# Kernel tuning notes

Measured on AMD Instinct MI355X. Metric: run time of the kernel, lower is better.

The kernel has to match this reference:

```python
import jax, jax.numpy as jnp
import numpy as np

N = 100_000      # nodes
F_IN = 256       # input features
HID = 256        # hidden dim
C = 40           # classes
E = 1_600_000    # edges
BN_EPS = 1e-5


def setup_inputs() -> dict:
    key = jax.random.key(0)
    ks = jax.random.split(key, 8)
    x = jax.random.normal(ks[0], (N, F_IN), dtype=jnp.float32)
    edge_index = jax.random.randint(ks[1], (2, E), 0, N)
    W1 = jax.random.normal(ks[2], (F_IN, HID), dtype=jnp.float32) / np.sqrt(F_IN)
    b1 = jnp.zeros((HID,), jnp.float32)
    gamma = jnp.ones((HID,), jnp.float32)
    beta = jnp.zeros((HID,), jnp.float32)
    W2 = jax.random.normal(ks[3], (HID, C), dtype=jnp.float32) / np.sqrt(HID)
    b2 = jnp.zeros((C,), jnp.float32)
    return {"x": x, "edge_index": edge_index, "W1": W1, "b1": b1,
            "gamma": gamma, "beta": beta, "W2": W2, "b2": b2}


def _gcn_propagate(h, src, dst, norm):
    # out[dst] += norm * h[src]   (symmetric-normalized aggregation, self-loops included)
    msg = norm[:, None] * h[src]                       # [E+N, D]
    return jax.ops.segment_sum(msg, dst, num_segments=N)


def reference(x, edge_index, W1, b1, gamma, beta, W2, b2):
    loops = jnp.arange(N, dtype=edge_index.dtype)
    src = jnp.concatenate([edge_index[0], loops])      # add self-loops (PyG GCNConv)
    dst = jnp.concatenate([edge_index[1], loops])
    deg = jax.ops.segment_sum(jnp.ones_like(dst, jnp.float32), dst, num_segments=N)
    dinv = jnp.where(deg > 0, jax.lax.rsqrt(deg), 0.0)
    norm = dinv[src] * dinv[dst]

    # Layer 1: GCNConv (linear without bias -> propagate -> + bias)
    h = _gcn_propagate(x @ W1, src, dst, norm) + b1    # [N, HID]
    # BatchNorm1d over nodes (training-style batch statistics, biased variance)
    mu = h.mean(axis=0)
    var = h.var(axis=0)
    h = (h - mu) * jax.lax.rsqrt(var + BN_EPS) * gamma + beta
    h = jax.nn.relu(h)                                 # dropout is identity in eval

    # Layer 2: GCNConv -> log_softmax
    out = _gcn_propagate(h @ W2, src, dst, norm) + b2  # [N, C]
    return jax.nn.log_softmax(out, axis=1)
```

## Files before the change

### kernel.cpp

```cpp
#include <hip/hip_runtime.h>
#include <math.h>

#define N_NODES 100000
#define F_IN    256
#define HID     256
#define C_OUT   40
#define N_EDGES 1600000
#define BN_EPS  1e-5f

#define SCAN_CHUNK  1024
#define SCAN_BLOCKS ((N_NODES + SCAN_CHUNK - 1) / SCAN_CHUNK)
#define CNT_BLOCKS  ((N_EDGES + 255) / 256)
#define NPASS 8
#define DRANGE (N_NODES / NPASS)

typedef __attribute__((ext_vector_type(8))) short short8;
typedef __attribute__((ext_vector_type(8))) unsigned short ushort8v;
typedef __attribute__((ext_vector_type(4))) float f32x4;

static __device__ __forceinline__ unsigned short f2bf(float f) {
    unsigned int u = __float_as_uint(f);
    unsigned int r = u + 0x7FFFu + ((u >> 16) & 1u);
    return (unsigned short)(r >> 16);
}
static __device__ __forceinline__ float bf2f(unsigned short b) {
    return __uint_as_float(((unsigned int)b) << 16);
}

__global__ void count_dst_castw(const int* __restrict__ dst, int* cnt,
                                const float* __restrict__ W1, const float* __restrict__ W2,
                                unsigned short* __restrict__ w1t, unsigned short* __restrict__ w2t) {
    int b = blockIdx.x, t = threadIdx.x;
    if (b < CNT_BLOCKS) {
        int i = b * 256 + t;
        if (i < N_EDGES) atomicAdd(&cnt[dst[i]], 1);
    } else if (b < CNT_BLOCKS + 256) {
        int n = b - CNT_BLOCKS;
        w1t[(size_t)n * 256 + t] = f2bf(W1[(size_t)t * 256 + n]);
    } else {
        int n = b - CNT_BLOCKS - 256;
        w2t[(size_t)n * 256 + t] = (n < C_OUT) ? f2bf(W2[(size_t)t * C_OUT + n]) : (unsigned short)0;
    }
}

__global__ __launch_bounds__(256) void scan_partial(const int* __restrict__ cnt,
                                                    int* blocksum) {
    __shared__ int red[256];
    int t = threadIdx.x;
    int base = blockIdx.x * SCAN_CHUNK + t * 4;
    int s = 0;
    if (base + 3 < N_NODES) {
        int4 c = *(const int4*)(cnt + base);
        s = c.x + c.y + c.z + c.w + 4;
    } else {
        for (int q = 0; q < 4; q++) if (base + q < N_NODES) s += cnt[base + q] + 1;
    }
    red[t] = s;
    __syncthreads();
    for (int off = 128; off > 0; off >>= 1) {
        if (t < off) red[t] += red[t + off];
        __syncthreads();
    }
    if (t == 0) blocksum[blockIdx.x] = red[0];
}

__global__ __launch_bounds__(128) void scan_blocksums(const int* __restrict__ blocksum,
                                                      int* blockoff, int* rowoff) {
    __shared__ int sm[128];
    int t = threadIdx.x;
    int v = (t < SCAN_BLOCKS) ? blocksum[t] : 0;
    sm[t] = v;
    __syncthreads();
    for (int off = 1; off < 128; off <<= 1) {
        int u = (t >= off) ? sm[t - off] : 0;
        __syncthreads();
        sm[t] += u;
        __syncthreads();
    }
    if (t < SCAN_BLOCKS) blockoff[t] = sm[t] - v;
    if (t == 0) rowoff[N_NODES] = N_EDGES + N_NODES;
}

__global__ __launch_bounds__(256) void scan_write_init(const int* __restrict__ cnt,
                                                       const int* __restrict__ blockoff,
                                                       int* rowoff, float* dinv,
                                                       int* cursor, int* csr) {
    __shared__ int red[256];
    int t = threadIdx.x;
    int base = blockIdx.x * SCAN_CHUNK + t * 4;
    int c[4] = {0, 0, 0, 0};
    if (base + 3 < N_NODES) {
        int4 cc = *(const int4*)(cnt + base);
        c[0] = cc.x + 1; c[1] = cc.y + 1; c[2] = cc.z + 1; c[3] = cc.w + 1;
    } else {
        for (int q = 0; q < 4; q++) c[q] = (base + q < N_NODES) ? cnt[base + q] + 1 : 0;
    }
    int s = c[0] + c[1] + c[2] + c[3];
    red[t] = s;
    __syncthreads();
    for (int off = 1; off < 256; off <<= 1) {
        int u = (t >= off) ? red[t - off] : 0;
        __syncthreads();
        red[t] += u;
        __syncthreads();
    }
    int run = blockoff[blockIdx.x] + red[t] - s;
    for (int q = 0; q < 4; q++) {
        int idx = base + q;
        if (idx < N_NODES) {
            rowoff[idx] = run;
            dinv[idx] = rsqrtf((float)c[q]);
            csr[run] = idx;
            cursor[idx] = 1;
            run += c[q];
        }
    }
}

__global__ void scatter_mp(const int* __restrict__ src,
                           const int* __restrict__ dst,
                           const int* __restrict__ rowoff,
                           int* cursor, int* csr) {
    int p = blockIdx.x / CNT_BLOCKS;
    int e = (blockIdx.x - p * CNT_BLOCKS) * 256 + threadIdx.x;
    if (e < N_EDGES) {
        int d = dst[e];
        if (d / DRANGE == p) {
            int pos = rowoff[d] + atomicAdd(&cursor[d], 1);
            csr[pos] = src[e];
        }
    }
}

#define LDK 56
__global__ __launch_bounds__(256) void gemm1_mfma(const float* __restrict__ x,
                                                  const unsigned short* __restrict__ w1t,
                                                  const float* __restrict__ dinv,
                                                  unsigned short* __restrict__ hs, int M) {
    __shared__ unsigned short As[64][LDK];
    __shared__ unsigned short Bs[256][LDK];
    int tid = threadIdx.x;
    int wave = tid >> 6, lane = tid & 63;
    int m0 = blockIdx.x * 64;
    f32x4 acc[4][4] = {};

    int ar = tid >> 2, ac = (tid & 3) * 8;
    int brow = tid;
    int gr = m0 + ar;
    bool rowok = gr < M;
    const float* xrow = x + (size_t)gr * 256 + ac;
    const unsigned short* wrow = w1t + (size_t)brow * 256;

    float4 pa = make_float4(0.f,0.f,0.f,0.f), pb = pa;
    if (rowok) { pa = *(const float4*)(xrow); pb = *(const float4*)(xrow + 4); }
    ushort8v rb0 = *(const ushort8v*)(wrow);
    ushort8v rb1 = *(const ushort8v*)(wrow + 8);
    ushort8v rb2 = *(const ushort8v*)(wrow + 16);
    ushort8v rb3 = *(const ushort8v*)(wrow + 24);

    for (int k0 = 0; k0 < 256; k0 += 32) {
        {
            ushort8v u;
            u[0] = f2bf(pa.x); u[1] = f2bf(pa.y); u[2] = f2bf(pa.z); u[3] = f2bf(pa.w);
            u[4] = f2bf(pb.x); u[5] = f2bf(pb.y); u[6] = f2bf(pb.z); u[7] = f2bf(pb.w);
            if (!rowok) {
#pragma unroll
                for (int q = 0; q < 8; q++) u[q] = 0;
            }
            *(ushort8v*)&As[ar][ac] = u;
        }
        *(ushort8v*)&Bs[brow][0]  = rb0;
        *(ushort8v*)&Bs[brow][8]  = rb1;
        *(ushort8v*)&Bs[brow][16] = rb2;
        *(ushort8v*)&Bs[brow][24] = rb3;
        __syncthreads();
        if (k0 + 32 < 256) {
            if (rowok) {
                pa = *(const float4*)(xrow + k0 + 32);
                pb = *(const float4*)(xrow + k0 + 36);
            }
            const unsigned short* p = wrow + k0 + 32;
            rb0 = *(const ushort8v*)(p);
            rb1 = *(const ushort8v*)(p + 8);
            rb2 = *(const ushort8v*)(p + 16);
            rb3 = *(const ushort8v*)(p + 24);
        }
        int fr = lane & 15, fk = (lane >> 4) * 8;
        short8 a[4], b[4];
#pragma unroll
        for (int mt = 0; mt < 4; mt++) a[mt] = *(short8*)&As[mt * 16 + fr][fk];
#pragma unroll
        for (int nt = 0; nt < 4; nt++) b[nt] = *(short8*)&Bs[wave * 64 + nt * 16 + fr][fk];
#pragma unroll
        for (int mt = 0; mt < 4; mt++)
#pragma unroll
            for (int nt = 0; nt < 4; nt++)
                acc[mt][nt] = __builtin_amdgcn_mfma_f32_16x16x32_bf16(a[mt], b[nt], acc[mt][nt], 0, 0, 0);
        __syncthreads();
    }
    int fr = lane & 15, fg = lane >> 4;
#pragma unroll
    for (int mt = 0; mt < 4; mt++) {
#pragma unroll
        for (int r = 0; r < 4; r++) {
            int row = m0 + mt * 16 + fg * 4 + r;
            if (row < M) {
                float dv = dinv[row];
#pragma unroll
                for (int nt = 0; nt < 4; nt++) {
                    int col = wave * 64 + nt * 16 + fr;
                    hs[(size_t)row * 256 + col] = f2bf(acc[mt][nt][r] * dv);
                }
            }
        }
    }
}

__global__ __launch_bounds__(256) void agg256(const int* __restrict__ rowoff,
                                              const int* __restrict__ csr,
                                              const unsigned short* __restrict__ hs,
                                              const float* __restrict__ dinv,
                                              unsigned short* __restrict__ hagg) {
    int g = blockIdx.x * blockDim.x + threadIdx.x;
    int wid = g >> 6, lane = g & 63;
    if (wid >= N_NODES) return;
    int half = lane >> 5;
    int c8 = (lane & 31) * 8;
    int beg = rowoff[wid], end = rowoff[wid + 1];
    float acc[8] = {0.f, 0.f, 0.f, 0.f, 0.f, 0.f, 0.f, 0.f};
    int j = beg;
    for (; j + 7 < end; j += 8) {
        int sx[4];
#pragma unroll
        for (int q = 0; q < 4; q++) sx[q] = csr[j + 2 * q + half];
        ushort8v u[4];
#pragma unroll
        for (int q = 0; q < 4; q++) u[q] = *(const ushort8v*)(hs + (size_t)sx[q] * 256 + c8);
#pragma unroll
        for (int q = 0; q < 4; q++)
#pragma unroll
            for (int e = 0; e < 8; e++) acc[e] += bf2f(u[q][e]);
    }
    for (; j + 1 < end; j += 2) {
        int s = csr[j + half];
        ushort8v u = *(const ushort8v*)(hs + (size_t)s * 256 + c8);
#pragma unroll
        for (int e = 0; e < 8; e++) acc[e] += bf2f(u[e]);
    }
    if (j < end && half == 0) {
        int s = csr[j];
        ushort8v u = *(const ushort8v*)(hs + (size_t)s * 256 + c8);
#pragma unroll
        for (int e = 0; e < 8; e++) acc[e] += bf2f(u[e]);
    }
#pragma unroll
    for (int e = 0; e < 8; e++) acc[e] += __shfl_xor(acc[e], 32);
    float dv = dinv[wid];
    if (half == 0) {
        ushort8v o;
#pragma unroll
        for (int e = 0; e < 8; e++) o[e] = f2bf(acc[e] * dv);
        *(ushort8v*)(hagg + (size_t)wid * 256 + c8) = o;
    }
}

#define BNS_BLOCKS 1024
__global__ __launch_bounds__(256) void bn_stats_v(const unsigned short* __restrict__ h,
                                                  float* musum, float* sqsum) {
    int tid = threadIdx.x;
    int wave = tid >> 6, lane = tid & 63;
    int half = lane >> 5;
    int c8 = (lane & 31) * 8;
    int gw = blockIdx.x * 4 + wave;
    float s[8] = {0.f,0.f,0.f,0.f,0.f,0.f,0.f,0.f};
    float q2[8] = {0.f,0.f,0.f,0.f,0.f,0.f,0.f,0.f};
    for (int r = gw * 2 + half; r < N_NODES; r += BNS_BLOCKS * 4 * 2) {
        ushort8v u = *(const ushort8v*)(h + (size_t)r * 256 + c8);
#pragma unroll
        for (int e = 0; e < 8; e++) {
            float v = bf2f(u[e]);
            s[e] += v; q2[e] += v * v;
        }
    }
#pragma unroll
    for (int e = 0; e < 8; e++) {
        s[e]  += __shfl_xor(s[e], 32);
        q2[e] += __shfl_xor(q2[e], 32);
    }
    __shared__ float sS[4][256];
    __shared__ float sQ[4][256];
    if (half == 0) {
#pragma unroll
        for (int e = 0; e < 8; e++) { sS[wave][c8 + e] = s[e]; sQ[wave][c8 + e] = q2[e]; }
    }
    __syncthreads();
    float a = sS[0][tid] + sS[1][tid] + sS[2][tid] + sS[3][tid];
    float b = sQ[0][tid] + sQ[1][tid] + sQ[2][tid] + sQ[3][tid];
    atomicAdd(&musum[tid], a);
    atomicAdd(&sqsum[tid], b);
}

#define LDB2 264
__global__ __launch_bounds__(256) void gemm2_mfma(const unsigned short* __restrict__ hagg,
                                                  const unsigned short* __restrict__ w2t,
                                                  const float* __restrict__ musum,
                                                  const float* __restrict__ sqsum,
                                                  const float* __restrict__ gamma,
                                                  const float* __restrict__ beta,
                                                  const float* __restrict__ dinv,
                                                  unsigned short* __restrict__ g2b, int M) {
    __shared__ unsigned short w2s[48][LDB2];
    __shared__ unsigned short As[64][40];
    __shared__ float ss[256], sh[256];
    int tid = threadIdx.x;
    int wave = tid >> 6, lane = tid & 63;
    int m0 = blockIdx.x * 64;

    for (int i = tid; i < 48 * 32; i += 256) {
        int rrow = i >> 5, c8 = (i & 31) * 8;
        *(ushort8v*)&w2s[rrow][c8] = *(const ushort8v*)(w2t + (size_t)rrow * 256 + c8);
    }
    {
        const float invN = 1.0f / N_NODES;
        float m = musum[tid] * invN;
        float var = sqsum[tid] * invN - m * m;
        float s = gamma[tid] * rsqrtf(var + BN_EPS);
        ss[tid] = s;
        sh[tid] = beta[tid] - m * s;
    }

    f32x4 acc[3] = {};
    int arow = tid >> 2, ac0 = (tid & 3) * 8;
    int fr = lane & 15, fk = (lane >> 4) * 8;

    for (int k0 = 0; k0 < 256; k0 += 32) {
        __syncthreads();
        {
            int gr = m0 + arow;
            ushort8v u;
            if (gr < M) {
                u = *(const ushort8v*)(hagg + (size_t)gr * 256 + k0 + ac0);
#pragma unroll
                for (int q = 0; q < 8; q++) {
                    int col = k0 + ac0 + q;
                    float v = bf2f(u[q]);
                    v = fmaxf(v * ss[col] + sh[col], 0.0f);
                    u[q] = f2bf(v);
                }
            } else {
#pragma unroll
                for (int q = 0; q < 8; q++) u[q] = 0;
            }
            *(ushort8v*)&As[arow][ac0] = u;
        }
        __syncthreads();
        short8 a = *(short8*)&As[wave * 16 + fr][fk];
#pragma unroll
        for (int nt = 0; nt < 3; nt++) {
            short8 b = *(short8*)&w2s[nt * 16 + fr][k0 + fk];
            acc[nt] = __builtin_amdgcn_mfma_f32_16x16x32_bf16(a, b, acc[nt], 0, 0, 0);
        }
    }
    int fg = lane >> 4;
#pragma unroll
    for (int nt = 0; nt < 3; nt++) {
        int col = nt * 16 + fr;
        if (col < C_OUT) {
#pragma unroll
            for (int r = 0; r < 4; r++) {
                int row = m0 + wave * 16 + fg * 4 + r;
                if (row < M) g2b[(size_t)row * C_OUT + col] = f2bf(acc[nt][r] * dinv[row]);
            }
        }
    }
}

__global__ __launch_bounds__(256) void agg40_logsm(const int* __restrict__ rowoff,
                                                   const int* __restrict__ csr,
                                                   const unsigned short* __restrict__ g2b,
                                                   const float* __restrict__ dinv,
                                                   const float* __restrict__ b2,
                                                   float* __restrict__ out) {
    int gi = blockIdx.x * blockDim.x + threadIdx.x;
    int wid = gi >> 6, lane = gi & 63;
    if (wid >= N_NODES) return;
    int g = lane / 10;
    int k4 = lane - g * 10;
    bool gact = lane < 60;
    int beg = rowoff[wid], end = rowoff[wid + 1];
    float a4[4] = {0.f, 0.f, 0.f, 0.f};
    for (int j = beg; j < end; j += 6) {
        int jj = j + g;
        if (gact && jj < end) {
            int s = csr[jj];
            ushort4 u = *(const ushort4*)(g2b + (size_t)s * C_OUT + k4 * 4);
            a4[0] += bf2f(u.x); a4[1] += bf2f(u.y);
            a4[2] += bf2f(u.z); a4[3] += bf2f(u.w);
        }
    }
#pragma unroll
    for (int e = 0; e < 4; e++) {
        float t0 = __shfl(a4[e], lane + 30);
        a4[e] += t0;
    }
#pragma unroll
    for (int e = 0; e < 4; e++) {
        float t1 = __shfl(a4[e], lane + 10);
        float t2 = __shfl(a4[e], lane + 20);
        a4[e] += t1 + t2;
    }
    bool act = lane < 10;
    float dvd = dinv[wid];
    float v[4];
    float mloc = -INFINITY;
#pragma unroll
    for (int e = 0; e < 4; e++) {
        v[e] = act ? a4[e] * dvd + b2[k4 * 4 + e] : -INFINITY;
        mloc = fmaxf(mloc, v[e]);
    }
#pragma unroll
    for (int o = 32; o > 0; o >>= 1) mloc = fmaxf(mloc, __shfl_xor(mloc, o));
    float sloc = 0.f;
    if (act) {
#pragma unroll
        for (int e = 0; e < 4; e++) sloc += __expf(v[e] - mloc);
    }
#pragma unroll
    for (int o = 32; o > 0; o >>= 1) sloc += __shfl_xor(sloc, o);
    float ls = __logf(sloc);
    if (act) {
        float4 o4 = make_float4(v[0] - mloc - ls, v[1] - mloc - ls,
                                v[2] - mloc - ls, v[3] - mloc - ls);
        *(float4*)(out + (size_t)wid * C_OUT + k4 * 4) = o4;
    }
}

extern "C" void kernel_launch(void* const* d_in, const int* in_sizes, int n_in,
                              void* d_out, int out_size, void* d_ws, size_t ws_size,
                              hipStream_t stream) {
    const float* x     = (const float*)d_in[0];
    const int*   ei    = (const int*)  d_in[1];
    const float* W1    = (const float*)d_in[2];
    const float* gamma = (const float*)d_in[4];
    const float* beta  = (const float*)d_in[5];
    const float* W2    = (const float*)d_in[6];
    const float* b2    = (const float*)d_in[7];
    float* out = (float*)d_out;

    const int* src = ei;
    const int* dst = ei + N_EDGES;

    unsigned short* hs    = (unsigned short*)d_ws;
    unsigned short* hagg  = hs + (size_t)N_NODES * 256;
    unsigned short* g2b   = hagg + (size_t)N_NODES * 256;
    float*          dinv  = (float*)(g2b + (size_t)N_NODES * C_OUT);
    int*            cnt   = (int*)(dinv + N_NODES);
    int*            rowoff= cnt + N_NODES;
    int*            cursor= rowoff + N_NODES + 1;
    int*            csr   = cursor + N_NODES;
    unsigned short* w1t   = (unsigned short*)(csr + N_EDGES + N_NODES);
    unsigned short* w2t   = w1t + 65536;
    float*          musum = (float*)(w2t + 48 * 256);
    float*          sqsum = musum + 256;
    int*            blocksum = (int*)(sqsum + 256);
    int*            blockoff = blocksum + 128;

    hipMemsetAsync(cnt, 0, N_NODES * sizeof(int), stream);
    hipMemsetAsync(musum, 0, 512 * sizeof(float), stream);

    count_dst_castw<<<CNT_BLOCKS + 256 + 48, 256, 0, stream>>>(dst, cnt, W1, W2, w1t, w2t);
    scan_partial<<<SCAN_BLOCKS, 256, 0, stream>>>(cnt, blocksum);
    scan_blocksums<<<1, 128, 0, stream>>>(blocksum, blockoff, rowoff);
    scan_write_init<<<SCAN_BLOCKS, 256, 0, stream>>>(cnt, blockoff, rowoff, dinv, cursor, csr);
    scatter_mp<<<NPASS * CNT_BLOCKS, 256, 0, stream>>>(src, dst, rowoff, cursor, csr);

    gemm1_mfma<<<(N_NODES + 63) / 64, 256, 0, stream>>>(x, w1t, dinv, hs, N_NODES);

    int aggblk = (int)(((size_t)N_NODES * 64 + 255) / 256);
    agg256<<<aggblk, 256, 0, stream>>>(rowoff, csr, hs, dinv, hagg);

    bn_stats_v<<<BNS_BLOCKS, 256, 0, stream>>>(hagg, musum, sqsum);

    gemm2_mfma<<<(N_NODES + 63) / 64, 256, 0, stream>>>(hagg, w2t, musum, sqsum, gamma, beta, dinv, g2b, N_NODES);

    agg40_logsm<<<aggblk, 256, 0, stream>>>(rowoff, csr, g2b, dinv, b2, out);
}
```

Measured before the change: 472.8 us.

## Slice 256-wide aggregation into 64-column slices and prefetch edges in agg40

The 256-feature aggregation now runs as four blocks per group of four nodes, each block covering a 64-column slice. Within a wave, 8 lanes cover the slice and 8 edges are gathered in parallel, followed by a shuffle reduction across edge groups. The intent is more memory-level parallelism per wave for low-degree nodes, and better cache locality since each slice's working set is smaller. The 40-class aggregation gains a software prefetch of the next edge batch. The cost is four times as many blocks, repeated rowoff and csr reads per slice, and an extra shuffle reduction.

```diff
diff --git a/kernel.cpp b/kernel.cpp
--- a/kernel.cpp
+++ b/kernel.cpp
@@ -13,6 +13,10 @@
 #define CNT_BLOCKS  ((N_EDGES + 255) / 256)
 #define NPASS 8
 #define DRANGE (N_NODES / NPASS)
+
+#define NSLICE 4
+#define AGG_NODE_GRP ((N_NODES + 3) / 4)
+#define AGG_S_BLOCKS (AGG_NODE_GRP * NSLICE)
 
 typedef __attribute__((ext_vector_type(8))) short short8;
 typedef __attribute__((ext_vector_type(8))) unsigned short ushort8v;
@@ -216,51 +220,41 @@
     }
 }
 
-__global__ __launch_bounds__(256) void agg256(const int* __restrict__ rowoff,
-                                              const int* __restrict__ csr,
-                                              const unsigned short* __restrict__ hs,
-                                              const float* __restrict__ dinv,
-                                              unsigned short* __restrict__ hagg) {
-    int g = blockIdx.x * blockDim.x + threadIdx.x;
-    int wid = g >> 6, lane = g & 63;
+__global__ __launch_bounds__(256) void agg256_sliced(const int* __restrict__ rowoff,
+                                                     const int* __restrict__ csr,
+                                                     const unsigned short* __restrict__ hs,
+                                                     const float* __restrict__ dinv,
+                                                     unsigned short* __restrict__ hagg) {
+    int slice = blockIdx.x & 3;
+    int wid = (blockIdx.x >> 2) * 4 + (threadIdx.x >> 6);
+    int lane = threadIdx.x & 63;
     if (wid >= N_NODES) return;
-    int half = lane >> 5;
-    int c8 = (lane & 31) * 8;
+    int sg = lane >> 3;
+    int co = (lane & 7) * 8;
+    const unsigned short* base = hs + slice * 64 + co;
     int beg = rowoff[wid], end = rowoff[wid + 1];
+    int jlim = end - 1;
     float acc[8] = {0.f, 0.f, 0.f, 0.f, 0.f, 0.f, 0.f, 0.f};
-    int j = beg;
-    for (; j + 7 < end; j += 8) {
-        int sx[4];
-#pragma unroll
-        for (int q = 0; q < 4; q++) sx[q] = csr[j + 2 * q + half];
-        ushort8v u[4];
-#pragma unroll
-        for (int q = 0; q < 4; q++) u[q] = *(const ushort8v*)(hs + (size_t)sx[q] * 256 + c8);
-#pragma unroll
-        for (int q = 0; q < 4; q++)
-#pragma unroll
-            for (int e = 0; e < 8; e++) acc[e] += bf2f(u[q][e]);
-    }
-    for (; j + 1 < end; j += 2) {
-        int s = csr[j + half];
-        ushort8v u = *(const ushort8v*)(hs + (size_t)s * 256 + c8);
-#pragma unroll
-        for (int e = 0; e < 8; e++) acc[e] += bf2f(u[e]);
-    }
-    if (j < end && half == 0) {
-        int s = csr[j];
-        ushort8v u = *(const ushort8v*)(hs + (size_t)s * 256 + c8);
-#pragma unroll
-        for (int e = 0; e < 8; e++) acc[e] += bf2f(u[e]);
-    }
-#pragma unroll
-    for (int e = 0; e < 8; e++) acc[e] += __shfl_xor(acc[e], 32);
-    float dv = dinv[wid];
-    if (half == 0) {
+    for (int j = beg; j < end; j += 8) {
+        int jj = j + sg;
+        int s = csr[min(jj, jlim)];
+        ushort8v u = *(const ushort8v*)(base + (size_t)s * 256);
+        if (jj < end) {
+#pragma unroll
+            for (int e = 0; e < 8; e++) acc[e] += bf2f(u[e]);
+        }
+    }
+#pragma unroll
+    for (int off = 8; off <= 32; off <<= 1) {
+#pragma unroll
+        for (int e = 0; e < 8; e++) acc[e] += __shfl_xor(acc[e], off);
+    }
+    if (sg == 0) {
+        float dv = dinv[wid];
         ushort8v o;
 #pragma unroll
         for (int e = 0; e < 8; e++) o[e] = f2bf(acc[e] * dv);
-        *(ushort8v*)(hagg + (size_t)wid * 256 + c8) = o;
+        *(ushort8v*)(hagg + (size_t)wid * 256 + slice * 64 + co) = o;
     }
 }
 
@@ -388,15 +382,25 @@
     int k4 = lane - g * 10;
     bool gact = lane < 60;
     int beg = rowoff[wid], end = rowoff[wid + 1];
+    int jlim = end - 1;
     float a4[4] = {0.f, 0.f, 0.f, 0.f};
-    for (int j = beg; j < end; j += 6) {
-        int jj = j + g;
-        if (gact && jj < end) {
-            int s = csr[jj];
-            ushort4 u = *(const ushort4*)(g2b + (size_t)s * C_OUT + k4 * 4);
-            a4[0] += bf2f(u.x); a4[1] += bf2f(u.y);
-            a4[2] += bf2f(u.z); a4[3] += bf2f(u.w);
-        }
+    int j = beg;
+    int s0 = csr[min(j + g, jlim)];
+    ushort4 u0 = *(const ushort4*)(g2b + (size_t)s0 * C_OUT + k4 * 4);
+    while (1) {
+        int jn = j + 6;
+        bool more = jn < end;
+        int s1 = 0; ushort4 u1;
+        if (more) {
+            s1 = csr[min(jn + g, jlim)];
+            u1 = *(const ushort4*)(g2b + (size_t)s1 * C_OUT + k4 * 4);
+        }
+        if (gact && j + g < end) {
+            a4[0] += bf2f(u0.x); a4[1] += bf2f(u0.y);
+            a4[2] += bf2f(u0.z); a4[3] += bf2f(u0.w);
+        }
+        if (!more) break;
+        u0 = u1; j = jn;
     }
 #pragma unroll
     for (int e = 0; e < 4; e++) {
@@ -476,12 +480,12 @@
 
     gemm1_mfma<<<(N_NODES + 63) / 64, 256, 0, stream>>>(x, w1t, dinv, hs, N_NODES);
 
+    agg256_sliced<<<AGG_S_BLOCKS, 256, 0, stream>>>(rowoff, csr, hs, dinv, hagg);
+
+    bn_stats_v<<<BNS_BLOCKS, 256, 0, stream>>>(hagg, musum, sqsum);
+
+    gemm2_mfma<<<(N_NODES + 63) / 64, 256, 0, stream>>>(hagg, w2t, musum, sqsum, gamma, beta, dinv, g2b, N_NODES);
+
     int aggblk = (int)(((size_t)N_NODES * 64 + 255) / 256);
-    agg256<<<aggblk, 256, 0, stream>>>(rowoff, csr, hs, dinv, hagg);
-
-    bn_stats_v<<<BNS_BLOCKS, 256, 0, stream>>>(hagg, musum, sqsum);
-
-    gemm2_mfma<<<(N_NODES + 63) / 64, 256, 0, stream>>>(hagg, w2t, musum, sqsum, gamma, beta, dinv, g2b, N_NODES);
-
     agg40_logsm<<<aggblk, 256, 0, stream>>>(rowoff, csr, g2b, dinv, b2, out);
 }
```

After: 527.8 us. 11.6% more time.
